# Kernel tuning notes

Measured on AMD Instinct MI355X. Metric: run time of the kernel, lower is better.

## Reference

```python
import jax, jax.numpy as jnp
import numpy as np
import math

H = 12          # num_attention_heads
DH = 64         # attention_head_size
LN_EPS = 1e-5


def layer_norm(x, gamma, beta):
    mu = jnp.mean(x, axis=-1, keepdims=True)
    var = jnp.mean(jnp.square(x - mu), axis=-1, keepdims=True)
    return (x - mu) * jax.lax.rsqrt(var + LN_EPS) * gamma + beta


def setup_inputs() -> dict:
    key = jax.random.key(0)
    ks = jax.random.split(key, 12)
    B, Lq, Lk, D = 4, 512, 512, 768
    s = 1.0 / math.sqrt(D)
    return {
        "hidden_states": jax.random.normal(ks[0], (B, Lq, D), jnp.float32),
        "context": jax.random.normal(ks[1], (B, Lk, D), jnp.float32),
        "attention_mask": jnp.zeros((B, 1, 1, Lk), jnp.float32),
        "graph_arc": jax.random.randint(ks[2], (B, Lq, Lk), 0, 3, jnp.int32),
        "Wq": jax.random.normal(ks[3], (D, D), jnp.float32) * s,
        "bq": jnp.zeros((D,), jnp.float32),
        "Wk": jax.random.normal(ks[4], (D, D), jnp.float32) * s,
        "bk": jnp.zeros((D,), jnp.float32),
        "Wv": jax.random.normal(ks[5], (D, D), jnp.float32) * s,
        "bv": jnp.zeros((D,), jnp.float32),
        "dpk_emb": jax.random.normal(ks[6], (3, DH), jnp.float32),
        "dpv_emb": jax.random.normal(ks[7], (3, DH), jnp.float32),
        "lnk_g": jnp.ones((DH,), jnp.float32),
        "lnk_b": jnp.zeros((DH,), jnp.float32),
        "lnv_g": jnp.ones((DH,), jnp.float32),
        "lnv_b": jnp.zeros((DH,), jnp.float32),
    }


def reference(hidden_states, context, attention_mask, graph_arc,
              Wq, bq, Wk, bk, Wv, bv,
              dpk_emb, dpv_emb, lnk_g, lnk_b, lnv_g, lnv_b):
    B, Lq, D = hidden_states.shape
    Lk = context.shape[1]

    def heads(x, L):  # [B,L,D] -> [B,H,L,dh]
        return x.reshape(B, L, H, DH).transpose(0, 2, 1, 3)

    q = heads(hidden_states @ Wq + bq, Lq)
    k = heads(context @ Wk + bk, Lk)
    v = heads(context @ Wv + bv, Lk)

    # relation embeddings per (query, key) pair: [B,Lq,Lk,dh]
    dp_keys = layer_norm(dpk_emb[graph_arc], lnk_g, lnk_b)
    dp_values = layer_norm(dpv_emb[graph_arc], lnv_g, lnv_b)

    scores = jnp.einsum('bhqd,bhkd->bhqk', q, k) / math.sqrt(DH)
    scores = scores + jnp.einsum('bhqd,bqkd->bhqk', q, dp_keys)
    scores = scores + attention_mask
    probs = jax.nn.softmax(scores, axis=-1)  # dropout p=0.0 -> identity

    ctx = jnp.einsum('bhqk,bhkd->bhqd', probs, v)
    ctx = ctx + jnp.einsum('bhqk,bqkd->bhqd', probs, dp_values)
    ctx = ctx.transpose(0, 2, 1, 3).reshape(B, Lq, D)
    return ctx
```

## Files before the change

### kernel.cpp

```cpp
#include <hip/hip_runtime.h>
#include <hip/hip_fp16.h>

#define NB 4
#define NH 12
#define DHD 64
#define LQ 512
#define LK 512
#define DM 768

typedef __attribute__((ext_vector_type(4))) _Float16 f16x4;
typedef __attribute__((ext_vector_type(8))) _Float16 f16x8;
typedef __attribute__((ext_vector_type(4))) float f32x4;

__global__ __launch_bounds__(256) void prep_kernel(
    const float* __restrict__ Wq, const float* __restrict__ Wk,
    const float* __restrict__ Wv,
    const float* __restrict__ dpk, const float* __restrict__ dpv,
    const float* __restrict__ gk, const float* __restrict__ bk,
    const float* __restrict__ gv, const float* __restrict__ bv,
    _Float16* __restrict__ WT, float* __restrict__ lnK, float* __restrict__ lnV)
{
    const int bid = blockIdx.x, t = threadIdx.x;
    if (bid < 432) {
        __shared__ float sT[64][65];
        int mat = bid / 144, tile = bid % 144;
        int k0 = (tile / 12) * 64, n0 = (tile % 12) * 64;
        const float* W = (mat == 0) ? Wq : (mat == 1) ? Wk : Wv;
        #pragma unroll
        for (int p = 0; p < 4; ++p) {
            int idx = t + p * 256;
            int ki = idx >> 4, nj = (idx & 15) * 4;
            float4 wv = *(const float4*)&W[(size_t)(k0 + ki) * DM + n0 + nj];
            sT[ki][nj + 0] = wv.x; sT[ki][nj + 1] = wv.y;
            sT[ki][nj + 2] = wv.z; sT[ki][nj + 3] = wv.w;
        }
        __syncthreads();
        _Float16* dst = WT + (size_t)mat * DM * DM;
        #pragma unroll
        for (int p = 0; p < 4; ++p) {
            int idx = t + p * 256;
            int nr = idx >> 4, kj = (idx & 15) * 4;
            f16x4 hv = { (_Float16)sT[kj + 0][nr], (_Float16)sT[kj + 1][nr],
                         (_Float16)sT[kj + 2][nr], (_Float16)sT[kj + 3][nr] };
            *(f16x4*)&dst[(size_t)(n0 + nr) * DM + k0 + kj] = hv;
        }
    } else if (t < 64) {
        int lane = t;
        for (int r = 0; r < 3; ++r) {
            {
                float x = dpk[r * DHD + lane];
                float s = x;
                #pragma unroll
                for (int o = 1; o < 64; o <<= 1) s += __shfl_xor(s, o);
                float mu = s * (1.0f / 64.0f);
                float d = x - mu;
                float v = d * d;
                #pragma unroll
                for (int o = 1; o < 64; o <<= 1) v += __shfl_xor(v, o);
                lnK[r * DHD + lane] =
                    (d * rsqrtf(v * (1.0f / 64.0f) + 1e-5f) * gk[lane] + bk[lane]) * 8.0f;
            }
            {
                float x = dpv[r * DHD + lane];
                float s = x;
                #pragma unroll
                for (int o = 1; o < 64; o <<= 1) s += __shfl_xor(s, o);
                float mu = s * (1.0f / 64.0f);
                float d = x - mu;
                float v = d * d;
                #pragma unroll
                for (int o = 1; o < 64; o <<= 1) v += __shfl_xor(v, o);
                lnV[r * DHD + lane] =
                    d * rsqrtf(v * (1.0f / 64.0f) + 1e-5f) * gv[lane] + bv[lane];
            }
        }
    }
}

__global__ __launch_bounds__(256) void qkv_mfma(
    const float* __restrict__ hidden, const float* __restrict__ context,
    const _Float16* __restrict__ WT,
    const float* __restrict__ bq, const float* __restrict__ bk,
    const float* __restrict__ bv,
    _Float16* __restrict__ Qh, _Float16* __restrict__ Kh,
    _Float16* __restrict__ VTh)
{
    __shared__ __align__(16) char smem[27648];
    _Float16 (*sA)[72]  = (_Float16(*)[72])smem;
    _Float16 (*sB)[72]  = (_Float16(*)[72])(smem + 9216);
    _Float16 (*sC)[136] = (_Float16(*)[136])smem;
    _Float16 (*sCV)[72] = (_Float16(*)[72])smem;

    const int t = threadIdx.x;
    const int w = t >> 6, lane = t & 63, g = lane >> 4, c16 = lane & 15;
    const int mat = blockIdx.y / 6, nt0 = blockIdx.y % 6;
    const int m0 = blockIdx.x * 64, n0 = nt0 * 128, head0 = nt0 * 2;
    const float* X     = (mat == 0) ? hidden : context;
    const _Float16* Wt = WT + (size_t)mat * DM * DM;
    const float* bias  = (mat == 0) ? bq : (mat == 1) ? bk : bv;

    f32x4 acc[4][2];
    #pragma unroll
    for (int mt = 0; mt < 4; ++mt)
        #pragma unroll
        for (int nt = 0; nt < 2; ++nt) acc[mt][nt] = (f32x4){0.f, 0.f, 0.f, 0.f};

    for (int kt = 0; kt < 12; ++kt) {
        __syncthreads();
        #pragma unroll
        for (int p = 0; p < 4; ++p) {
            int idx = t + p * 256;
            int row = idx >> 4, c4 = idx & 15;
            float4 xv = *(const float4*)&X[(size_t)(m0 + row) * DM + kt * 64 + c4 * 4];
            f16x4 hv = { (_Float16)xv.x, (_Float16)xv.y,
                         (_Float16)xv.z, (_Float16)xv.w };
            *(f16x4*)&sA[row][c4 * 4] = hv;
        }
        #pragma unroll
        for (int p = 0; p < 4; ++p) {
            int idx = t + p * 256;
            int n = idx >> 3, c8 = idx & 7;
            *(f16x8*)&sB[n][c8 * 8] =
                *(const f16x8*)&Wt[(size_t)(n0 + n) * DM + kt * 64 + c8 * 8];
        }
        __syncthreads();
        #pragma unroll
        for (int kh = 0; kh < 2; ++kh) {
            f16x8 af[4], bf[2];
            #pragma unroll
            for (int mt = 0; mt < 4; ++mt)
                af[mt] = *(const f16x8*)&sA[mt * 16 + c16][kh * 32 + 8 * g];
            #pragma unroll
            for (int nt = 0; nt < 2; ++nt)
                bf[nt] = *(const f16x8*)&sB[w * 32 + nt * 16 + c16][kh * 32 + 8 * g];
            #pragma unroll
            for (int mt = 0; mt < 4; ++mt)
                #pragma unroll
                for (int nt = 0; nt < 2; ++nt)
                    acc[mt][nt] = __builtin_amdgcn_mfma_f32_16x16x32_f16(
                        af[mt], bf[nt], acc[mt][nt], 0, 0, 0);
        }
    }

    const float sc = (mat == 0) ? 0.125f : 1.0f;
    float bb[2];
    #pragma unroll
    for (int nt = 0; nt < 2; ++nt)
        bb[nt] = bias[n0 + w * 32 + nt * 16 + c16] * sc;
    __syncthreads();

    const int bbat = m0 >> 9, l0 = m0 & 511;
    if (mat < 2) {
        #pragma unroll
        for (int mt = 0; mt < 4; ++mt)
            #pragma unroll
            for (int nt = 0; nt < 2; ++nt)
                #pragma unroll
                for (int r = 0; r < 4; ++r)
                    sC[mt * 16 + 4 * g + r][w * 32 + nt * 16 + c16] =
                        (_Float16)(acc[mt][nt][r] * sc + bb[nt]);
        __syncthreads();
        _Float16* dst = (mat == 0) ? Qh : Kh;
        #pragma unroll
        for (int p = 0; p < 4; ++p) {
            int idx = t + p * 256;
            int row = idx >> 4, cg = idx & 15;
            int hl = cg >> 3, d8 = cg & 7;
            *(f16x8*)&dst[((size_t)(bbat * NH + head0 + hl) * LQ + l0 + row) * DHD + d8 * 8] =
                *(const f16x8*)&sC[row][cg * 8];
        }
    } else {
        #pragma unroll
        for (int mt = 0; mt < 4; ++mt)
            #pragma unroll
            for (int nt = 0; nt < 2; ++nt)
                #pragma unroll
                for (int r = 0; r < 4; ++r)
                    sCV[w * 32 + nt * 16 + c16][mt * 16 + 4 * g + r] =
                        (_Float16)(acc[mt][nt][r] + bb[nt]);
        __syncthreads();
        #pragma unroll
        for (int p = 0; p < 4; ++p) {
            int idx = t + p * 256;
            int n = idx >> 3, c8 = idx & 7;
            *(f16x8*)&VTh[((size_t)(bbat * NH + head0 + (n >> 6)) * DHD + (n & 63)) * LK
                          + l0 + c8 * 8] = *(const f16x8*)&sCV[n][c8 * 8];
        }
    }
}

__global__ __launch_bounds__(256) void attn_mfma(
    const _Float16* __restrict__ Qh, const _Float16* __restrict__ Kh,
    const _Float16* __restrict__ VTh, const float* __restrict__ maskp,
    const int* __restrict__ garc, const float* __restrict__ lnK,
    const float* __restrict__ lnV, float* __restrict__ outp)
{
    __shared__ __align__(16) _Float16 sP[32][520];
    __shared__ unsigned char sArc[32][512];
    __shared__ float sTb[32][4];
    __shared__ float sMax[4][32];
    __shared__ float sStat[4][32][4];
    __shared__ float sFin[32][4];

    const int t = threadIdx.x;
    const int w = t >> 6, lane = t & 63, g = lane >> 4, c16 = lane & 15;
    const int bx = blockIdx.x;
    const int qt = bx & 15, h = (bx >> 4) % NH, b = bx / (16 * NH);
    const int q0 = qt * 32;
    const int kw = w * 128;

    const _Float16* Qb = Qh + ((size_t)(b * NH + h) * LQ) * DHD;
    const _Float16* Kb = Kh + ((size_t)(b * NH + h) * LK) * DHD;
    const _Float16* Vb = VTh + ((size_t)(b * NH + h) * DHD) * LK;

    const int* garcRow = garc + ((size_t)(b * LQ + q0)) * LK;
    unsigned char* sArcFlat = &sArc[0][0];
    #pragma unroll
    for (int p = 0; p < 16; ++p) {
        int idx = t + p * 256;
        int4 a4 = *(const int4*)&garcRow[idx * 4];
        uchar4 u = { (unsigned char)a4.x, (unsigned char)a4.y,
                     (unsigned char)a4.z, (unsigned char)a4.w };
        *(uchar4*)&sArcFlat[idx * 4] = u;
    }
    if (t < 192) {
        int q = t / 6, rem = t % 6, rr = rem >> 1, part = rem & 1;
        float a = 0.f;
        const _Float16* qrow = Qb + (q0 + q) * DHD;
        #pragma unroll
        for (int d0 = 0; d0 < 32; ++d0) {
            int d = part * 32 + d0;
            a += (float)qrow[d] * lnK[rr * 64 + d];
        }
        a += __shfl_xor(a, 1);
        if (part == 0) sTb[q][rr] = a;
    }
    f16x8 qa[2][2];
    #pragma unroll
    for (int qg = 0; qg < 2; ++qg) {
        qa[qg][0] = *(const f16x8*)&Qb[(q0 + 16 * qg + c16) * DHD + 8 * g];
        qa[qg][1] = *(const f16x8*)&Qb[(q0 + 16 * qg + c16) * DHD + 32 + 8 * g];
    }
    __syncthreads();

    f32x4 c[8][2];
    int aPack[8][2];
    float rm[2][4];
    #pragma unroll
    for (int qg = 0; qg < 2; ++qg)
        #pragma unroll
        for (int r = 0; r < 4; ++r) rm[qg][r] = -1e30f;
    #pragma unroll
    for (int tt = 0; tt < 8; ++tt) {
        int kg = kw + tt * 16 + c16;
        f16x8 kb0 = *(const f16x8*)&Kb[kg * DHD + 8 * g];
        f16x8 kb1 = *(const f16x8*)&Kb[kg * DHD + 32 + 8 * g];
        float mv = maskp[b * LK + kg];
        #pragma unroll
        for (int qg = 0; qg < 2; ++qg) {
            f32x4 s = (f32x4){0.f, 0.f, 0.f, 0.f};
            s = __builtin_amdgcn_mfma_f32_16x16x32_f16(qa[qg][0], kb0, s, 0, 0, 0);
            s = __builtin_amdgcn_mfma_f32_16x16x32_f16(qa[qg][1], kb1, s, 0, 0, 0);
            int ap = 0;
            #pragma unroll
            for (int r = 0; r < 4; ++r) {
                int qrow = 16 * qg + 4 * g + r;
                int a = sArc[qrow][kg];
                ap |= a << (8 * r);
                float sv = s[r] + sTb[qrow][a] + mv;
                s[r] = sv;
                rm[qg][r] = fmaxf(rm[qg][r], sv);
            }
            c[tt][qg] = s;
            aPack[tt][qg] = ap;
        }
    }

    #pragma unroll
    for (int qg = 0; qg < 2; ++qg)
        #pragma unroll
        for (int r = 0; r < 4; ++r) {
            float m = rm[qg][r];
            m = fmaxf(m, __shfl_xor(m, 1));
            m = fmaxf(m, __shfl_xor(m, 2));
            m = fmaxf(m, __shfl_xor(m, 4));
            m = fmaxf(m, __shfl_xor(m, 8));
            rm[qg][r] = m;
        }
    if (c16 == 0)
        #pragma unroll
        for (int qg = 0; qg < 2; ++qg)
            #pragma unroll
            for (int r = 0; r < 4; ++r) sMax[w][16 * qg + 4 * g + r] = rm[qg][r];
    __syncthreads();
    float Mr[2][4];
    #pragma unroll
    for (int qg = 0; qg < 2; ++qg)
        #pragma unroll
        for (int r = 0; r < 4; ++r) {
            int q = 16 * qg + 4 * g + r;
            Mr[qg][r] = fmaxf(fmaxf(sMax[0][q], sMax[1][q]),
                              fmaxf(sMax[2][q], sMax[3][q]));
        }

    float rs[2][4], b0s[2][4], b1s[2][4], b2s[2][4];
    #pragma unroll
    for (int qg = 0; qg < 2; ++qg)
        #pragma unroll
        for (int r = 0; r < 4; ++r) {
            rs[qg][r] = 0.f; b0s[qg][r] = 0.f; b1s[qg][r] = 0.f; b2s[qg][r] = 0.f;
        }
    #pragma unroll
    for (int tt = 0; tt < 8; ++tt) {
        int kg = kw + tt * 16 + c16;
        #pragma unroll
        for (int qg = 0; qg < 2; ++qg)
            #pragma unroll
            for (int r = 0; r < 4; ++r) {
                float e = __expf(c[tt][qg][r] - Mr[qg][r]);
                int a = (aPack[tt][qg] >> (8 * r)) & 255;
                rs[qg][r] += e;
                b0s[qg][r] += (a == 0) ? e : 0.f;
                b1s[qg][r] += (a == 1) ? e : 0.f;
                b2s[qg][r] += (a == 2) ? e : 0.f;
                sP[16 * qg + 4 * g + r][kg] = (_Float16)e;
            }
    }
    #pragma unroll
    for (int qg = 0; qg < 2; ++qg)
        #pragma unroll
        for (int r = 0; r < 4; ++r) {
            #pragma unroll
            for (int o = 1; o < 16; o <<= 1) {
                rs[qg][r]  += __shfl_xor(rs[qg][r], o);
                b0s[qg][r] += __shfl_xor(b0s[qg][r], o);
                b1s[qg][r] += __shfl_xor(b1s[qg][r], o);
                b2s[qg][r] += __shfl_xor(b2s[qg][r], o);
            }
        }
    if (c16 == 0)
        #pragma unroll
        for (int qg = 0; qg < 2; ++qg)
            #pragma unroll
            for (int r = 0; r < 4; ++r) {
                float4 v = make_float4(rs[qg][r], b0s[qg][r], b1s[qg][r], b2s[qg][r]);
                *(float4*)&sStat[w][16 * qg + 4 * g + r][0] = v;
            }
    __syncthreads();
    if (t < 32) {
        float4 tot = make_float4(0.f, 0.f, 0.f, 0.f);
        #pragma unroll
        for (int ww = 0; ww < 4; ++ww) {
            float4 v = *(const float4*)&sStat[ww][t][0];
            tot.x += v.x; tot.y += v.y; tot.z += v.z; tot.w += v.w;
        }
        sFin[t][0] = 1.0f / tot.x;
        sFin[t][1] = tot.y; sFin[t][2] = tot.z; sFin[t][3] = tot.w;
    }

    f32x4 o[2] = {(f32x4){0.f, 0.f, 0.f, 0.f}, (f32x4){0.f, 0.f, 0.f, 0.f}};
    const _Float16* vrow = Vb + (size_t)(w * 16 + c16) * LK;
    #pragma unroll
    for (int ktile = 0; ktile < 16; ++ktile) {
        f16x8 vb = *(const f16x8*)&vrow[ktile * 32 + 8 * g];
        #pragma unroll
        for (int qg = 0; qg < 2; ++qg) {
            f16x8 pa = *(const f16x8*)&sP[16 * qg + c16][ktile * 32 + 8 * g];
            o[qg] = __builtin_amdgcn_mfma_f32_16x16x32_f16(pa, vb, o[qg], 0, 0, 0);
        }
    }
    __syncthreads();

    int d = w * 16 + c16;
    float lv0 = lnV[d], lv1 = lnV[64 + d], lv2 = lnV[128 + d];
    #pragma unroll
    for (int qg = 0; qg < 2; ++qg)
        #pragma unroll
        for (int r = 0; r < 4; ++r) {
            int q = 16 * qg + 4 * g + r;
            float4 st = *(const float4*)&sFin[q][0];
            float val = (o[qg][r] + st.y * lv0 + st.z * lv1 + st.w * lv2) * st.x;
            outp[((size_t)(b * LQ + q0 + q)) * DM + h * DHD + d] = val;
        }
}

extern "C" void kernel_launch(void* const* d_in, const int* in_sizes, int n_in,
                              void* d_out, int out_size, void* d_ws, size_t ws_size,
                              hipStream_t stream) {
    const float* hidden  = (const float*)d_in[0];
    const float* context = (const float*)d_in[1];
    const float* mask    = (const float*)d_in[2];
    const int*   garc    = (const int*)d_in[3];
    const float* Wq = (const float*)d_in[4];
    const float* bq = (const float*)d_in[5];
    const float* Wk = (const float*)d_in[6];
    const float* bk = (const float*)d_in[7];
    const float* Wv = (const float*)d_in[8];
    const float* bv = (const float*)d_in[9];
    const float* dpk  = (const float*)d_in[10];
    const float* dpv  = (const float*)d_in[11];
    const float* lnkg = (const float*)d_in[12];
    const float* lnkb = (const float*)d_in[13];
    const float* lnvg = (const float*)d_in[14];
    const float* lnvb = (const float*)d_in[15];
    float* out = (float*)d_out;

    const size_t perT = (size_t)NB * NH * LQ * DHD;
    _Float16* Qh  = (_Float16*)d_ws;
    _Float16* Kh  = Qh + perT;
    _Float16* VTh = Kh + perT;
    _Float16* WT  = VTh + perT;
    float* lnK = (float*)(WT + (size_t)3 * DM * DM);
    float* lnV = lnK + 192;

    prep_kernel<<<433, 256, 0, stream>>>(Wq, Wk, Wv, dpk, dpv,
                                         lnkg, lnkb, lnvg, lnvb, WT, lnK, lnV);
    qkv_mfma<<<dim3(32, 18), 256, 0, stream>>>(hidden, context, WT,
                                               bq, bk, bv, Qh, Kh, VTh);
    attn_mfma<<<768, 256, 0, stream>>>(Qh, Kh, VTh, mask, garc, lnK, lnV, out);
}
```

Measured before the change: 142.1 us.

## Retile QKV GEMM to 64x96 blocks and pack arc indices as 2-bit words

The QKV projection now uses 64x96 output tiles with a 2x2 wave layout, giving 768 blocks instead of 576 for better CU fill on the machine. The attention kernel packs graph_arc values into 2-bit fields (16 per 32-bit word, padded stride) to cut shared memory and bank conflicts. It also vectorizes the q·lnK dot product and derives the softmax row sum from the three per-arc bucket sums, dropping one accumulator and its shuffles. The retiled GEMM has a smaller reuse footprint per block, and the sum-from-buckets trick relies on arc values always being 0..2.

Measured after the change: 139.1 us. -2.1%, faster.

```diff
diff --git a/kernel.cpp b/kernel.cpp
--- a/kernel.cpp
+++ b/kernel.cpp
@@ -85,25 +85,26 @@
     _Float16* __restrict__ Qh, _Float16* __restrict__ Kh,
     _Float16* __restrict__ VTh)
 {
-    __shared__ __align__(16) char smem[27648];
+    __shared__ __align__(16) char smem[23040];
     _Float16 (*sA)[72]  = (_Float16(*)[72])smem;
     _Float16 (*sB)[72]  = (_Float16(*)[72])(smem + 9216);
-    _Float16 (*sC)[136] = (_Float16(*)[136])smem;
+    _Float16 (*sC)[104] = (_Float16(*)[104])smem;
     _Float16 (*sCV)[72] = (_Float16(*)[72])smem;
 
     const int t = threadIdx.x;
     const int w = t >> 6, lane = t & 63, g = lane >> 4, c16 = lane & 15;
-    const int mat = blockIdx.y / 6, nt0 = blockIdx.y % 6;
-    const int m0 = blockIdx.x * 64, n0 = nt0 * 128, head0 = nt0 * 2;
+    const int wm = w >> 1, wn = w & 1;
+    const int mat = blockIdx.y / 8, nt0 = blockIdx.y % 8;
+    const int m0 = blockIdx.x * 64, n0 = nt0 * 96;
     const float* X     = (mat == 0) ? hidden : context;
     const _Float16* Wt = WT + (size_t)mat * DM * DM;
     const float* bias  = (mat == 0) ? bq : (mat == 1) ? bk : bv;
 
-    f32x4 acc[4][2];
-    #pragma unroll
-    for (int mt = 0; mt < 4; ++mt)
-        #pragma unroll
-        for (int nt = 0; nt < 2; ++nt) acc[mt][nt] = (f32x4){0.f, 0.f, 0.f, 0.f};
+    f32x4 acc[2][3];
+    #pragma unroll
+    for (int mt = 0; mt < 2; ++mt)
+        #pragma unroll
+        for (int nt = 0; nt < 3; ++nt) acc[mt][nt] = (f32x4){0.f, 0.f, 0.f, 0.f};
 
     for (int kt = 0; kt < 12; ++kt) {
         __syncthreads();
@@ -117,7 +118,7 @@
             *(f16x4*)&sA[row][c4 * 4] = hv;
         }
         #pragma unroll
-        for (int p = 0; p < 4; ++p) {
+        for (int p = 0; p < 3; ++p) {
             int idx = t + p * 256;
             int n = idx >> 3, c8 = idx & 7;
             *(f16x8*)&sB[n][c8 * 8] =
@@ -126,64 +127,64 @@
         __syncthreads();
         #pragma unroll
         for (int kh = 0; kh < 2; ++kh) {
-            f16x8 af[4], bf[2];
-            #pragma unroll
-            for (int mt = 0; mt < 4; ++mt)
-                af[mt] = *(const f16x8*)&sA[mt * 16 + c16][kh * 32 + 8 * g];
-            #pragma unroll
-            for (int nt = 0; nt < 2; ++nt)
-                bf[nt] = *(const f16x8*)&sB[w * 32 + nt * 16 + c16][kh * 32 + 8 * g];
-            #pragma unroll
-            for (int mt = 0; mt < 4; ++mt)
-                #pragma unroll
-                for (int nt = 0; nt < 2; ++nt)
+            f16x8 af[2], bf[3];
+            #pragma unroll
+            for (int mt = 0; mt < 2; ++mt)
+                af[mt] = *(const f16x8*)&sA[wm * 32 + mt * 16 + c16][kh * 32 + 8 * g];
+            #pragma unroll
+            for (int nt = 0; nt < 3; ++nt)
+                bf[nt] = *(const f16x8*)&sB[wn * 48 + nt * 16 + c16][kh * 32 + 8 * g];
+            #pragma unroll
+            for (int mt = 0; mt < 2; ++mt)
+                #pragma unroll
+                for (int nt = 0; nt < 3; ++nt)
                     acc[mt][nt] = __builtin_amdgcn_mfma_f32_16x16x32_f16(
                         af[mt], bf[nt], acc[mt][nt], 0, 0, 0);
         }
     }
 
     const float sc = (mat == 0) ? 0.125f : 1.0f;
-    float bb[2];
-    #pragma unroll
-    for (int nt = 0; nt < 2; ++nt)
-        bb[nt] = bias[n0 + w * 32 + nt * 16 + c16] * sc;
+    float bb[3];
+    #pragma unroll
+    for (int nt = 0; nt < 3; ++nt)
+        bb[nt] = bias[n0 + wn * 48 + nt * 16 + c16] * sc;
     __syncthreads();
 
     const int bbat = m0 >> 9, l0 = m0 & 511;
     if (mat < 2) {
         #pragma unroll
-        for (int mt = 0; mt < 4; ++mt)
-            #pragma unroll
-            for (int nt = 0; nt < 2; ++nt)
+        for (int mt = 0; mt < 2; ++mt)
+            #pragma unroll
+            for (int nt = 0; nt < 3; ++nt)
                 #pragma unroll
                 for (int r = 0; r < 4; ++r)
-                    sC[mt * 16 + 4 * g + r][w * 32 + nt * 16 + c16] =
+                    sC[wm * 32 + mt * 16 + 4 * g + r][wn * 48 + nt * 16 + c16] =
                         (_Float16)(acc[mt][nt][r] * sc + bb[nt]);
         __syncthreads();
         _Float16* dst = (mat == 0) ? Qh : Kh;
-        #pragma unroll
-        for (int p = 0; p < 4; ++p) {
-            int idx = t + p * 256;
-            int row = idx >> 4, cg = idx & 15;
-            int hl = cg >> 3, d8 = cg & 7;
-            *(f16x8*)&dst[((size_t)(bbat * NH + head0 + hl) * LQ + l0 + row) * DHD + d8 * 8] =
-                *(const f16x8*)&sC[row][cg * 8];
+        int row = t >> 2, qc = t & 3;
+        #pragma unroll
+        for (int j = 0; j < 3; ++j) {
+            int col = qc * 24 + j * 8;
+            int hd = (n0 + col) >> 6, d8 = (n0 + col) & 63;
+            *(f16x8*)&dst[((size_t)(bbat * NH + hd) * LQ + l0 + row) * DHD + d8] =
+                *(const f16x8*)&sC[row][col];
         }
     } else {
         #pragma unroll
-        for (int mt = 0; mt < 4; ++mt)
-            #pragma unroll
-            for (int nt = 0; nt < 2; ++nt)
+        for (int mt = 0; mt < 2; ++mt)
+            #pragma unroll
+            for (int nt = 0; nt < 3; ++nt)
                 #pragma unroll
                 for (int r = 0; r < 4; ++r)
-                    sCV[w * 32 + nt * 16 + c16][mt * 16 + 4 * g + r] =
+                    sCV[wn * 48 + nt * 16 + c16][wm * 32 + mt * 16 + 4 * g + r] =
                         (_Float16)(acc[mt][nt][r] + bb[nt]);
         __syncthreads();
         #pragma unroll
-        for (int p = 0; p < 4; ++p) {
+        for (int p = 0; p < 3; ++p) {
             int idx = t + p * 256;
             int n = idx >> 3, c8 = idx & 7;
-            *(f16x8*)&VTh[((size_t)(bbat * NH + head0 + (n >> 6)) * DHD + (n & 63)) * LK
+            *(f16x8*)&VTh[((size_t)(bbat * NH + ((n0 + n) >> 6)) * DHD + ((n0 + n) & 63)) * LK
                           + l0 + c8 * 8] = *(const f16x8*)&sCV[n][c8 * 8];
         }
     }
@@ -196,7 +197,7 @@
     const float* __restrict__ lnV, float* __restrict__ outp)
 {
     __shared__ __align__(16) _Float16 sP[32][520];
-    __shared__ unsigned char sArc[32][512];
+    __shared__ unsigned int sArcW[32 * 33];
     __shared__ float sTb[32][4];
     __shared__ float sMax[4][32];
     __shared__ float sStat[4][32][4];
@@ -214,23 +215,36 @@
     const _Float16* Vb = VTh + ((size_t)(b * NH + h) * DHD) * LK;
 
     const int* garcRow = garc + ((size_t)(b * LQ + q0)) * LK;
-    unsigned char* sArcFlat = &sArc[0][0];
-    #pragma unroll
-    for (int p = 0; p < 16; ++p) {
+    #pragma unroll
+    for (int p = 0; p < 4; ++p) {
         int idx = t + p * 256;
-        int4 a4 = *(const int4*)&garcRow[idx * 4];
-        uchar4 u = { (unsigned char)a4.x, (unsigned char)a4.y,
-                     (unsigned char)a4.z, (unsigned char)a4.w };
-        *(uchar4*)&sArcFlat[idx * 4] = u;
+        int row = idx >> 5, wd = idx & 31;
+        const int4* src = (const int4*)&garcRow[idx * 16];
+        unsigned int u = 0;
+        #pragma unroll
+        for (int j = 0; j < 4; ++j) {
+            int4 a4 = src[j];
+            u |= (unsigned int)a4.x << (j * 8 + 0);
+            u |= (unsigned int)a4.y << (j * 8 + 2);
+            u |= (unsigned int)a4.z << (j * 8 + 4);
+            u |= (unsigned int)a4.w << (j * 8 + 6);
+        }
+        sArcW[row * 33 + wd] = u;
     }
     if (t < 192) {
         int q = t / 6, rem = t % 6, rr = rem >> 1, part = rem & 1;
+        const _Float16* qp = Qb + (size_t)(q0 + q) * DHD + part * 32;
+        const float* lp = lnK + rr * 64 + part * 32;
         float a = 0.f;
-        const _Float16* qrow = Qb + (q0 + q) * DHD;
-        #pragma unroll
-        for (int d0 = 0; d0 < 32; ++d0) {
-            int d = part * 32 + d0;
-            a += (float)qrow[d] * lnK[rr * 64 + d];
+        #pragma unroll
+        for (int j = 0; j < 4; ++j) {
+            f16x8 qv = *(const f16x8*)&qp[j * 8];
+            float4 l0 = *(const float4*)&lp[j * 8];
+            float4 l1 = *(const float4*)&lp[j * 8 + 4];
+            a += (float)qv[0] * l0.x + (float)qv[1] * l0.y
+               + (float)qv[2] * l0.z + (float)qv[3] * l0.w
+               + (float)qv[4] * l1.x + (float)qv[5] * l1.y
+               + (float)qv[6] * l1.z + (float)qv[7] * l1.w;
         }
         a += __shfl_xor(a, 1);
         if (part == 0) sTb[q][rr] = a;
@@ -246,6 +260,7 @@
     f32x4 c[8][2];
     int aPack[8][2];
     float rm[2][4];
+    const int sh = c16 * 2;
     #pragma unroll
     for (int qg = 0; qg < 2; ++qg)
         #pragma unroll
@@ -256,6 +271,7 @@
         f16x8 kb0 = *(const f16x8*)&Kb[kg * DHD + 8 * g];
         f16x8 kb1 = *(const f16x8*)&Kb[kg * DHD + 32 + 8 * g];
         float mv = maskp[b * LK + kg];
+        const int wb = w * 8 + tt;
         #pragma unroll
         for (int qg = 0; qg < 2; ++qg) {
             f32x4 s = (f32x4){0.f, 0.f, 0.f, 0.f};
@@ -265,7 +281,7 @@
             #pragma unroll
             for (int r = 0; r < 4; ++r) {
                 int qrow = 16 * qg + 4 * g + r;
-                int a = sArc[qrow][kg];
+                int a = (int)((sArcW[qrow * 33 + wb] >> sh) & 3u);
                 ap |= a << (8 * r);
                 float sv = s[r] + sTb[qrow][a] + mv;
                 s[r] = sv;
@@ -303,12 +319,12 @@
                               fmaxf(sMax[2][q], sMax[3][q]));
         }
 
-    float rs[2][4], b0s[2][4], b1s[2][4], b2s[2][4];
+    float b0s[2][4], b1s[2][4], b2s[2][4];
     #pragma unroll
     for (int qg = 0; qg < 2; ++qg)
         #pragma unroll
         for (int r = 0; r < 4; ++r) {
-            rs[qg][r] = 0.f; b0s[qg][r] = 0.f; b1s[qg][r] = 0.f; b2s[qg][r] = 0.f;
+            b0s[qg][r] = 0.f; b1s[qg][r] = 0.f; b2s[qg][r] = 0.f;
         }
     #pragma unroll
     for (int tt = 0; tt < 8; ++tt) {
@@ -319,7 +335,6 @@
             for (int r = 0; r < 4; ++r) {
                 float e = __expf(c[tt][qg][r] - Mr[qg][r]);
                 int a = (aPack[tt][qg] >> (8 * r)) & 255;
-                rs[qg][r] += e;
                 b0s[qg][r] += (a == 0) ? e : 0.f;
                 b1s[qg][r] += (a == 1) ? e : 0.f;
                 b2s[qg][r] += (a == 2) ? e : 0.f;
@@ -332,7 +347,6 @@
         for (int r = 0; r < 4; ++r) {
             #pragma unroll
             for (int o = 1; o < 16; o <<= 1) {
-                rs[qg][r]  += __shfl_xor(rs[qg][r], o);
                 b0s[qg][r] += __shfl_xor(b0s[qg][r], o);
                 b1s[qg][r] += __shfl_xor(b1s[qg][r], o);
                 b2s[qg][r] += __shfl_xor(b2s[qg][r], o);
@@ -343,7 +357,7 @@
         for (int qg = 0; qg < 2; ++qg)
             #pragma unroll
             for (int r = 0; r < 4; ++r) {
-                float4 v = make_float4(rs[qg][r], b0s[qg][r], b1s[qg][r], b2s[qg][r]);
+                float4 v = make_float4(b0s[qg][r], b1s[qg][r], b2s[qg][r], 0.f);
                 *(float4*)&sStat[w][16 * qg + 4 * g + r][0] = v;
             }
     __syncthreads();
@@ -352,10 +366,10 @@
         #pragma unroll
         for (int ww = 0; ww < 4; ++ww) {
             float4 v = *(const float4*)&sStat[ww][t][0];
-            tot.x += v.x; tot.y += v.y; tot.z += v.z; tot.w += v.w;
-        }
-        sFin[t][0] = 1.0f / tot.x;
-        sFin[t][1] = tot.y; sFin[t][2] = tot.z; sFin[t][3] = tot.w;
+            tot.x += v.x; tot.y += v.y; tot.z += v.z;
+        }
+        sFin[t][0] = 1.0f / (tot.x + tot.y + tot.z);
+        sFin[t][1] = tot.x; sFin[t][2] = tot.y; sFin[t][3] = tot.z;
     }
 
     f32x4 o[2] = {(f32x4){0.f, 0.f, 0.f, 0.f}, (f32x4){0.f, 0.f, 0.f, 0.f}};
@@ -415,7 +429,7 @@
 
     prep_kernel<<<433, 256, 0, stream>>>(Wq, Wk, Wv, dpk, dpv,
                                          lnkg, lnkb, lnvg, lnvb, WT, lnK, lnV);
-    qkv_mfma<<<dim3(32, 18), 256, 0, stream>>>(hidden, context, WT,
+    qkv_mfma<<<dim3(32, 24), 256, 0, stream>>>(hidden, context, WT,
                                                bq, bk, bv, Qh, Kh, VTh);
     attn_mfma<<<768, 256, 0, stream>>>(Qh, Kh, VTh, mask, garc, lnK, lnV, out);
 }
```
